# Performance work log

Hardware: AMD Instinct MI355X
Metric: run time of the kernel (lower is better)

## Reference

```python
import jax, jax.numpy as jnp
import numpy as np

SAMPLE_RATE = 44100
NUM_FILTERS = 3
FREQ_LO, FREQ_HI = 100.0, 3000.0
Q_LO, Q_HI = 1.0, 5.0
GAIN_LO, GAIN_HI = -24.0, 24.0


def _center_freqs():
    # power_ratio(i/N, f_lo, f_hi) = f_lo * (f_hi/f_lo)**(i/N)
    return [FREQ_LO * (FREQ_HI / FREQ_LO) ** (i / NUM_FILTERS) for i in range(NUM_FILTERS)]


def setup_inputs() -> dict:
    key = jax.random.key(0)
    k1, k2, k3 = jax.random.split(key, 3)
    audio = jax.random.normal(k1, (32, 441000), dtype=jnp.float32)  # [B, T]
    # Q sampled like power_ratio(u, q_lo, q_hi) = q_lo*(q_hi/q_lo)**u
    u = jax.random.uniform(k2, (NUM_FILTERS,), dtype=jnp.float32)
    qs = Q_LO * (Q_HI / Q_LO) ** u
    gains = jax.random.uniform(k3, (NUM_FILTERS,), dtype=jnp.float32,
                               minval=GAIN_LO, maxval=GAIN_HI)
    return {"audio": audio, "qs": qs, "gains": gains}


def _biquad(x, b0, b1, b2, a1, a2):
    """Direct-form-I biquad over time axis. x: [B, T]; coeffs normalized by a0."""
    B = x.shape[0]
    z = jnp.zeros((B,), x.dtype)

    def step(carry, xn):
        x1, x2, y1, y2 = carry
        yn = b0 * xn + b1 * x1 + b2 * x2 - a1 * y1 - a2 * y2
        return (xn, x1, yn, y1), yn

    _, y = jax.lax.scan(step, (z, z, z, z), x.T)  # scan over T
    return y.T


def _peaking_eq(audio, center_freq, gain, Q):
    # torchaudio.functional.equalizer_biquad coefficients
    w0 = 2.0 * jnp.pi * center_freq / SAMPLE_RATE
    alpha = jnp.sin(w0) / (2.0 * Q)
    A = jnp.exp(gain / 40.0 * jnp.log(10.0))  # 10**(gain/40)
    b0 = 1.0 + alpha * A
    b1 = -2.0 * jnp.cos(w0)
    b2 = 1.0 - alpha * A
    a0 = 1.0 + alpha / A
    a1 = -2.0 * jnp.cos(w0)
    a2 = 1.0 - alpha / A
    return _biquad(audio, b0 / a0, b1 / a0, b2 / a0, a1 / a0, a2 / a0)


def reference(audio, qs, gains):
    cfs = _center_freqs()
    for i in range(NUM_FILTERS):
        audio = _peaking_eq(audio, cfs[i], gains[i], qs[i])
    return audio
```

## Files before the change

### kernel.cpp

```cpp
#include <hip/hip_runtime.h>
#include <math.h>

#define SR      44100.0
#define T_LEN   441000
#define B_ROWS  32
#define CHUNK   32
#define NCH     13782
#define WPR     216
#define NWAVE   (B_ROWS * WPR)
#define NBLK    (NWAVE / 4)
#define NSEG    8
#define SEGCH   1724

#define WS_COEF 0
#define WS_W    16
#define WS_G    64
#define WS_V    128
#define WS_T    512
#define WS_E    2048
#define WS_F    1574912

typedef __attribute__((address_space(1))) const void gconst_t;
typedef __attribute__((address_space(3))) void lds_t;
#define GL2LDS(gp, lp) __builtin_amdgcn_global_load_lds((gconst_t*)(gp), (lds_t*)(lp), 16, 0, 0)


__device__ __forceinline__ void mm6(const double* X, const double* Y, double* Z, int t) {
  if (t < 36) {
    int i = t / 6, j = t % 6;
    double s = 0.0;
    #pragma unroll
    for (int k = 0; k < 6; k++) s += X[i*6+k] * Y[k*6+j];
    Z[t] = s;
  }
}

__global__ __launch_bounds__(64) void k0_setup(const float* __restrict__ qs,
                                               const float* __restrict__ gains,
                                               float* __restrict__ ws) {
  __shared__ double dco[3][5];
  __shared__ double M0[36], M1[36];
  __shared__ double Vd[10][36];
  int t = threadIdx.x;
  if (t < 3) {
    int f = t;
    double cf = 100.0 * exp(log(30.0) * (double)f / 3.0);
    double w0 = 2.0 * M_PI * cf / SR;
    double alpha = sin(w0) / (2.0 * (double)qs[f]);
    double Ag = exp((double)gains[f] * (2.302585092994045684 / 40.0));
    double a0 = 1.0 + alpha / Ag;
    dco[f][0] = (1.0 + alpha * Ag) / a0;
    dco[f][1] = (-2.0 * cos(w0)) / a0;
    dco[f][2] = (1.0 - alpha * Ag) / a0;
    dco[f][3] = (-2.0 * cos(w0)) / a0;
    dco[f][4] = (1.0 - alpha / Ag) / a0;
  }
  __syncthreads();
  if (t < 15) ws[WS_COEF + t] = (float)dco[t/5][t%5];
  if (t == 0) {
    double u[7] = {0,0,0,0,0,0,1};
    for (int f = 0; f < 3; f++) {
      double b0=dco[f][0], b1=dco[f][1], b2=dco[f][2], a1=dco[f][3], a2=dco[f][4];
      double yv[7], s1p[7], s2p[7];
      for (int i = 0; i < 7; i++) {
        yv[i]  = b0 * u[i] + ((i == 2*f)   ? 1.0 : 0.0);
        s1p[i] = b1 * u[i] + ((i == 2*f+1) ? 1.0 : 0.0) - a1 * yv[i];
        s2p[i] = b2 * u[i] - a2 * yv[i];
      }
      for (int i = 0; i < 6; i++) { M0[(2*f)*6+i] = s1p[i]; M0[(2*f+1)*6+i] = s2p[i]; }
      for (int i = 0; i < 7; i++) u[i] = yv[i];
    }
  }
  __syncthreads();
  double* cur = M0; double* oth = M1;
  for (int s = 0; s < 5; s++) {
    mm6(cur, cur, oth, t); __syncthreads();
    double* tm = cur; cur = oth; oth = tm;
  }
  if (t < 36) ws[WS_W + t] = (float)cur[t];
  mm6(cur, cur, Vd[0], t); __syncthreads();
  for (int k = 1; k < 10; k++) { mm6(Vd[k-1], Vd[k-1], Vd[k], t); __syncthreads(); }
  if (t < 36) for (int k = 0; k < 10; k++) ws[WS_V + k*36 + t] = (float)Vd[k][t];
  mm6(Vd[1], Vd[2], oth, t); __syncthreads();
  mm6(oth, Vd[3], cur, t); __syncthreads();
  mm6(cur, Vd[4], oth, t); __syncthreads();
  mm6(oth, Vd[6], cur, t); __syncthreads();
  mm6(cur, Vd[8], oth, t); __syncthreads();
  mm6(oth, Vd[9], cur, t); __syncthreads();
  if (t < 36) ws[WS_G + t] = (float)cur[t];
}


#define LOAD_COEFS(cf) \
  const float b00=cf[0],b10=cf[1],b20=cf[2],a10=cf[3],a20=cf[4]; \
  const float b01=cf[5],b11=cf[6],b21=cf[7],a11=cf[8],a21=cf[9]; \
  const float b02=cf[10],b12=cf[11],b22=cf[12],a12=cf[13],a22=cf[14];

#define CASCADE_STEP(xx) do { \
    float y1 = fmaf(b00, (xx), s11); \
    s11 = fmaf(-a10, y1, fmaf(b10, (xx), s21)); \
    s21 = fmaf(-a20, y1, b20 * (xx)); \
    float y2 = fmaf(b01, y1, s12); \
    s12 = fmaf(-a11, y2, fmaf(b11, y1, s22)); \
    s22 = fmaf(-a21, y2, b21 * y1); \
    y3 = fmaf(b02, y2, s13); \
    s13 = fmaf(-a12, y3, fmaf(b12, y2, s23)); \
    s23 = fmaf(-a22, y3, b22 * y2); \
  } while (0)



__global__ __launch_bounds__(256) void k1_states(const float* __restrict__ x,
                                                 float* __restrict__ ws) {
  __shared__ float lds[4 * 2048];
  int wib = threadIdx.x >> 6, lane = threadIdx.x & 63;
  int gw = blockIdx.x * 4 + wib;
  int row = gw / WPR, wci = gw % WPR;
  long rowbase = (long)row * T_LEN;
  int s0 = wci << 11;
  int span4 = (min(2048, T_LEN - s0)) >> 2;
  const float4* xp = (const float4*)(x + rowbase + s0);
  float* slab = lds + (wib << 11);
  if (span4 == 512) {
    #pragma unroll
    for (int i = 0; i < 8; i++) {
      int s = (i << 6) + lane;
      int g = (s & ~7) | ((s & 7) ^ ((s >> 3) & 7));
      GL2LDS(xp + g, slab + (i << 8));
    }
  } else {
    #pragma unroll
    for (int i = 0; i < 8; i++) {
      int s = (i << 6) + lane;
      int g = (s & ~7) | ((s & 7) ^ ((s >> 3) & 7));
      if (g < span4) GL2LDS(xp + g, slab + (i << 8));
    }
  }
  __syncthreads();
  int ci = (wci << 6) + lane;
  if (ci < NCH) {
    const float* cf = ws + WS_COEF;
    LOAD_COEFS(cf);
    int rem = min(CHUNK, T_LEN - (ci << 5));
    int n4 = rem >> 2;
    const float* rowp = slab + (lane << 5);
    int xr = lane & 7;
    float s11=0,s21=0,s12=0,s22=0,s13=0,s23=0, y3;
    if (n4 == 8) {
      #pragma unroll
      for (int j4 = 0; j4 < 8; j4++) {
        float4 v = *(const float4*)(rowp + ((j4 ^ xr) << 2));
        CASCADE_STEP(v.x); CASCADE_STEP(v.y); CASCADE_STEP(v.z); CASCADE_STEP(v.w);
      }
    } else {
      for (int j4 = 0; j4 < n4; j4++) {
        float4 v = *(const float4*)(rowp + ((j4 ^ xr) << 2));
        CASCADE_STEP(v.x); CASCADE_STEP(v.y); CASCADE_STEP(v.z); CASCADE_STEP(v.w);
      }
    }
    (void)y3;
    float* F = ws + WS_F + ((long)row * NCH + ci) * 6;
    F[0]=s11; F[1]=s21; F[2]=s12; F[3]=s22; F[4]=s13; F[5]=s23;
  }
}


__global__ __launch_bounds__(1024) void k2a(float* __restrict__ ws) {
  int seg = blockIdx.x & 7, row = blockIdx.x >> 3, t = threadIdx.x;
  __shared__ float bufA[1024][7], bufB[1024][7];
  __shared__ float sW[36], sV[10][36];
  for (int i = t; i < 36; i += 1024) sW[i] = ws[WS_W + i];
  for (int i = t; i < 360; i += 1024) sV[i/36][i%36] = ws[WS_V + i];
  int segstart = seg * SEGCH;
  int nch = min(SEGCH, NCH - segstart);
  int nact = nch >> 1;
  __syncthreads();
  const float* F = ws + WS_F + ((long)row * NCH + segstart) * 6;
  float v[6] = {0,0,0,0,0,0};
  if (t < nact) {
    #pragma unroll
    for (int c = 0; c < 2; c++) {
      const float* Fj = F + (long)(2*t + c) * 6;
      float nv[6];
      #pragma unroll
      for (int i = 0; i < 6; i++) {
        float s = Fj[i];
        #pragma unroll
        for (int k = 0; k < 6; k++) s = fmaf(sW[i*6+k], v[k], s);
        nv[i] = s;
      }
      #pragma unroll
      for (int i = 0; i < 6; i++) v[i] = nv[i];
    }
  }
  #pragma unroll
  for (int i = 0; i < 6; i++) bufA[t][i] = v[i];
  __syncthreads();
  float (*src)[7] = bufA, (*dst)[7] = bufB;
  for (int k = 0; k < 10; k++) {
    int d = 1 << k;
    float nv[6];
    if (t >= d) {
      #pragma unroll
      for (int i = 0; i < 6; i++) {
        float s = src[t][i];
        #pragma unroll
        for (int kk = 0; kk < 6; kk++) s = fmaf(sV[k][i*6+kk], src[t-d][kk], s);
        nv[i] = s;
      }
    } else {
      #pragma unroll
      for (int i = 0; i < 6; i++) nv[i] = src[t][i];
    }
    #pragma unroll
    for (int i = 0; i < 6; i++) dst[t][i] = nv[i];
    __syncthreads();
    float (*tm)[7] = src; src = dst; dst = tm;
  }
  float* Ep = ws + WS_E + ((long)blockIdx.x * 1024 + t) * 6;
  if (t > 0) {
    #pragma unroll
    for (int i = 0; i < 6; i++) Ep[i] = src[t-1][i];
  } else {
    #pragma unroll
    for (int i = 0; i < 6; i++) Ep[i] = 0.0f;
  }
  if (t == nact - 1) {
    float* Tp = ws + WS_T + (long)blockIdx.x * 6;
    #pragma unroll
    for (int i = 0; i < 6; i++) Tp[i] = src[t][i];
  }
}


__global__ __launch_bounds__(1024) void k2c(float* __restrict__ ws) {
  int seg = blockIdx.x & 7, row = blockIdx.x >> 3, t = threadIdx.x;
  __shared__ float sW[36], sG[36], sV[10][36], sT[8][6], sO[6];
  for (int i = t; i < 36; i += 1024) { sW[i] = ws[WS_W + i]; sG[i] = ws[WS_G + i]; }
  for (int i = t; i < 360; i += 1024) sV[i/36][i%36] = ws[WS_V + i];
  if (t < 48) sT[t/6][t%6] = ws[WS_T + ((long)(row*8) + t/6) * 6 + t%6];
  __syncthreads();
  if (t == 0) {
    float o[6] = {0,0,0,0,0,0};
    for (int s2 = 0; s2 < seg; s2++) {
      float no[6];
      #pragma unroll
      for (int i = 0; i < 6; i++) {
        float s = sT[s2][i];
        #pragma unroll
        for (int k = 0; k < 6; k++) s = fmaf(sG[i*6+k], o[k], s);
        no[i] = s;
      }
      #pragma unroll
      for (int i = 0; i < 6; i++) o[i] = no[i];
    }
    #pragma unroll
    for (int i = 0; i < 6; i++) sO[i] = o[i];
  }
  __syncthreads();
  int segstart = seg * SEGCH;
  int nch = min(SEGCH, NCH - segstart);
  int nact = nch >> 1;
  if (t < nact) {
    float e[6];
    #pragma unroll
    for (int i = 0; i < 6; i++) e[i] = sO[i];
    for (int k = 0; k < 10; k++) {
      if ((t >> k) & 1) {
        float ne[6];
        #pragma unroll
        for (int i = 0; i < 6; i++) {
          float s = 0.0f;
          #pragma unroll
          for (int kk = 0; kk < 6; kk++) s = fmaf(sV[k][i*6+kk], e[kk], s);
          ne[i] = s;
        }
        #pragma unroll
        for (int i = 0; i < 6; i++) e[i] = ne[i];
      }
    }
    const float* Er = ws + WS_E + ((long)blockIdx.x * 1024 + t) * 6;
    #pragma unroll
    for (int i = 0; i < 6; i++) e[i] += Er[i];
    float* Fj = ws + WS_F + ((long)row * NCH + segstart + 2*t) * 6;
    #pragma unroll
    for (int c = 0; c < 2; c++) {
      float nv[6];
      #pragma unroll
      for (int i = 0; i < 6; i++) {
        float s = Fj[c*6 + i];
        #pragma unroll
        for (int k = 0; k < 6; k++) s = fmaf(sW[i*6+k], e[k], s);
        nv[i] = s;
      }
      #pragma unroll
      for (int i = 0; i < 6; i++) { Fj[c*6 + i] = e[i]; e[i] = nv[i]; }
    }
  }
}


__global__ __launch_bounds__(256) void k3_emit(const float* __restrict__ x,
                                               float* __restrict__ y,
                                               const float* __restrict__ ws) {
  __shared__ float lds[4 * 2048];
  int wib = threadIdx.x >> 6, lane = threadIdx.x & 63;
  int gw = blockIdx.x * 4 + wib;
  int row = gw / WPR, wci = gw % WPR;
  long rowbase = (long)row * T_LEN;
  int s0 = wci << 11;
  int span4 = (min(2048, T_LEN - s0)) >> 2;
  const float4* xp = (const float4*)(x + rowbase + s0);
  float* slab = lds + (wib << 11);
  if (span4 == 512) {
    #pragma unroll
    for (int i = 0; i < 8; i++) {
      int s = (i << 6) + lane;
      int g = (s & ~7) | ((s & 7) ^ ((s >> 3) & 7));
      GL2LDS(xp + g, slab + (i << 8));
    }
  } else {
    #pragma unroll
    for (int i = 0; i < 8; i++) {
      int s = (i << 6) + lane;
      int g = (s & ~7) | ((s & 7) ^ ((s >> 3) & 7));
      if (g < span4) GL2LDS(xp + g, slab + (i << 8));
    }
  }
  int ci = (wci << 6) + lane;
  float e0=0,e1=0,e2=0,e3=0,e4=0,e5=0;
  if (ci < NCH) {
    const float* E = ws + WS_F + ((long)row * NCH + ci) * 6;
    e0=E[0]; e1=E[1]; e2=E[2]; e3=E[3]; e4=E[4]; e5=E[5];
  }
  __syncthreads();
  if (ci < NCH) {
    const float* cf = ws + WS_COEF;
    LOAD_COEFS(cf);
    float s11=e0, s21=e1, s12=e2, s22=e3, s13=e4, s23=e5;
    int rem = min(CHUNK, T_LEN - (ci << 5));
    int n4 = rem >> 2;
    float* rowp = slab + (lane << 5);
    int xr = lane & 7;
    float y3;
    if (n4 == 8) {
      #pragma unroll
      for (int j4 = 0; j4 < 8; j4++) {
        float* p = rowp + ((j4 ^ xr) << 2);
        float4 v = *(const float4*)p;
        float4 o;
        CASCADE_STEP(v.x); o.x = y3;
        CASCADE_STEP(v.y); o.y = y3;
        CASCADE_STEP(v.z); o.z = y3;
        CASCADE_STEP(v.w); o.w = y3;
        *(float4*)p = o;
      }
    } else {
      for (int j4 = 0; j4 < n4; j4++) {
        float* p = rowp + ((j4 ^ xr) << 2);
        float4 v = *(const float4*)p;
        float4 o;
        CASCADE_STEP(v.x); o.x = y3;
        CASCADE_STEP(v.y); o.y = y3;
        CASCADE_STEP(v.z); o.z = y3;
        CASCADE_STEP(v.w); o.w = y3;
        *(float4*)p = o;
      }
    }
  }
  __syncthreads();
  float4* yp = (float4*)(y + rowbase + s0);
  if (span4 == 512) {
    #pragma unroll
    for (int i = 0; i < 8; i++) {
      int g = (i << 6) + lane;
      int s = (g & ~7) | ((g & 7) ^ ((g >> 3) & 7));
      yp[g] = *(const float4*)(slab + (s << 2));
    }
  } else {
    #pragma unroll
    for (int i = 0; i < 8; i++) {
      int g = (i << 6) + lane;
      int s = (g & ~7) | ((g & 7) ^ ((g >> 3) & 7));
      if (g < span4) yp[g] = *(const float4*)(slab + (s << 2));
    }
  }
}

extern "C" void kernel_launch(void* const* d_in, const int* in_sizes, int n_in,
                              void* d_out, int out_size, void* d_ws, size_t ws_size,
                              hipStream_t stream) {
  const float* audio = (const float*)d_in[0];
  const float* qs    = (const float*)d_in[1];
  const float* gains = (const float*)d_in[2];
  float* out = (float*)d_out;
  float* ws  = (float*)d_ws;

  hipLaunchKernelGGL(k0_setup, dim3(1), dim3(64), 0, stream, qs, gains, ws);
  hipLaunchKernelGGL(k1_states, dim3(NBLK), dim3(256), 0, stream, audio, ws);
  hipLaunchKernelGGL(k2a, dim3(B_ROWS * NSEG), dim3(1024), 0, stream, ws);
  hipLaunchKernelGGL(k2c, dim3(B_ROWS * NSEG), dim3(1024), 0, stream, ws);
  hipLaunchKernelGGL(k3_emit, dim3(NBLK), dim3(256), 0, stream, audio, out, ws);
}
```

Baseline: 64.98 us.

## Collapse five-kernel pipeline to three by fusing setup and per-row scan

Removes the separate setup kernel: the biquad coefficients are now recomputed per block in the state and emit kernels, and the transition-matrix powers are computed inside the scan kernel. The two segmented scan kernels are merged into one kernel with one block per row, where each thread serially folds 14 chunks, runs a 10-round Hillis-Steele scan, then writes the corrected states back. This cuts two kernel launches and the cross-segment fixup. In exchange only 32 blocks run the scan, with longer serial per-thread loops and redundant double-precision matrix setup in every block.

```diff
diff --git a/kernel.cpp b/kernel.cpp
--- a/kernel.cpp
+++ b/kernel.cpp
@@ -9,87 +9,31 @@
 #define WPR     216
 #define NWAVE   (B_ROWS * WPR)
 #define NBLK    (NWAVE / 4)
-#define NSEG    8
-#define SEGCH   1724
-
-#define WS_COEF 0
-#define WS_W    16
-#define WS_G    64
-#define WS_V    128
-#define WS_T    512
-#define WS_E    2048
-#define WS_F    1574912
+#define SPAN    14
+#define ROUNDS  10
+
+#define WS_F    0
 
 typedef __attribute__((address_space(1))) const void gconst_t;
 typedef __attribute__((address_space(3))) void lds_t;
 #define GL2LDS(gp, lp) __builtin_amdgcn_global_load_lds((gconst_t*)(gp), (lds_t*)(lp), 16, 0, 0)
 
 
-__device__ __forceinline__ void mm6(const double* X, const double* Y, double* Z, int t) {
-  if (t < 36) {
-    int i = t / 6, j = t % 6;
-    double s = 0.0;
-    #pragma unroll
-    for (int k = 0; k < 6; k++) s += X[i*6+k] * Y[k*6+j];
-    Z[t] = s;
-  }
-}
-
-__global__ __launch_bounds__(64) void k0_setup(const float* __restrict__ qs,
-                                               const float* __restrict__ gains,
-                                               float* __restrict__ ws) {
-  __shared__ double dco[3][5];
-  __shared__ double M0[36], M1[36];
-  __shared__ double Vd[10][36];
-  int t = threadIdx.x;
-  if (t < 3) {
-    int f = t;
-    double cf = 100.0 * exp(log(30.0) * (double)f / 3.0);
-    double w0 = 2.0 * M_PI * cf / SR;
-    double alpha = sin(w0) / (2.0 * (double)qs[f]);
-    double Ag = exp((double)gains[f] * (2.302585092994045684 / 40.0));
-    double a0 = 1.0 + alpha / Ag;
-    dco[f][0] = (1.0 + alpha * Ag) / a0;
-    dco[f][1] = (-2.0 * cos(w0)) / a0;
-    dco[f][2] = (1.0 - alpha * Ag) / a0;
-    dco[f][3] = (-2.0 * cos(w0)) / a0;
-    dco[f][4] = (1.0 - alpha / Ag) / a0;
-  }
-  __syncthreads();
-  if (t < 15) ws[WS_COEF + t] = (float)dco[t/5][t%5];
-  if (t == 0) {
-    double u[7] = {0,0,0,0,0,0,1};
-    for (int f = 0; f < 3; f++) {
-      double b0=dco[f][0], b1=dco[f][1], b2=dco[f][2], a1=dco[f][3], a2=dco[f][4];
-      double yv[7], s1p[7], s2p[7];
-      for (int i = 0; i < 7; i++) {
-        yv[i]  = b0 * u[i] + ((i == 2*f)   ? 1.0 : 0.0);
-        s1p[i] = b1 * u[i] + ((i == 2*f+1) ? 1.0 : 0.0) - a1 * yv[i];
-        s2p[i] = b2 * u[i] - a2 * yv[i];
-      }
-      for (int i = 0; i < 6; i++) { M0[(2*f)*6+i] = s1p[i]; M0[(2*f+1)*6+i] = s2p[i]; }
-      for (int i = 0; i < 7; i++) u[i] = yv[i];
-    }
-  }
-  __syncthreads();
-  double* cur = M0; double* oth = M1;
-  for (int s = 0; s < 5; s++) {
-    mm6(cur, cur, oth, t); __syncthreads();
-    double* tm = cur; cur = oth; oth = tm;
-  }
-  if (t < 36) ws[WS_W + t] = (float)cur[t];
-  mm6(cur, cur, Vd[0], t); __syncthreads();
-  for (int k = 1; k < 10; k++) { mm6(Vd[k-1], Vd[k-1], Vd[k], t); __syncthreads(); }
-  if (t < 36) for (int k = 0; k < 10; k++) ws[WS_V + k*36 + t] = (float)Vd[k][t];
-  mm6(Vd[1], Vd[2], oth, t); __syncthreads();
-  mm6(oth, Vd[3], cur, t); __syncthreads();
-  mm6(cur, Vd[4], oth, t); __syncthreads();
-  mm6(oth, Vd[6], cur, t); __syncthreads();
-  mm6(cur, Vd[8], oth, t); __syncthreads();
-  mm6(oth, Vd[9], cur, t); __syncthreads();
-  if (t < 36) ws[WS_G + t] = (float)cur[t];
-}
-
+#define COMPUTE_COEFS_TO_LDS(scoef, qs, gains) do { \
+    if (threadIdx.x < 3) { \
+      int f = threadIdx.x; \
+      double cfq = 100.0 * exp(log(30.0) * (double)f / 3.0); \
+      double w0 = 2.0 * M_PI * cfq / SR; \
+      double alpha = sin(w0) / (2.0 * (double)qs[f]); \
+      double Ag = exp((double)gains[f] * (2.302585092994045684 / 40.0)); \
+      double a0 = 1.0 + alpha / Ag; \
+      scoef[f*5+0] = (float)((1.0 + alpha * Ag) / a0); \
+      scoef[f*5+1] = (float)((-2.0 * cos(w0)) / a0); \
+      scoef[f*5+2] = (float)((1.0 - alpha * Ag) / a0); \
+      scoef[f*5+3] = (float)((-2.0 * cos(w0)) / a0); \
+      scoef[f*5+4] = (float)((1.0 - alpha / Ag) / a0); \
+    } \
+  } while (0)
 
 #define LOAD_COEFS(cf) \
   const float b00=cf[0],b10=cf[1],b20=cf[2],a10=cf[3],a20=cf[4]; \
@@ -110,9 +54,12 @@
 
 
 
-__global__ __launch_bounds__(256) void k1_states(const float* __restrict__ x,
+__global__ __launch_bounds__(256) void kA_states(const float* __restrict__ x,
+                                                 const float* __restrict__ qs,
+                                                 const float* __restrict__ gains,
                                                  float* __restrict__ ws) {
   __shared__ float lds[4 * 2048];
+  __shared__ float scoef[16];
   int wib = threadIdx.x >> 6, lane = threadIdx.x & 63;
   int gw = blockIdx.x * 4 + wib;
   int row = gw / WPR, wci = gw % WPR;
@@ -136,11 +83,11 @@
       if (g < span4) GL2LDS(xp + g, slab + (i << 8));
     }
   }
+  COMPUTE_COEFS_TO_LDS(scoef, qs, gains);
   __syncthreads();
   int ci = (wci << 6) + lane;
   if (ci < NCH) {
-    const float* cf = ws + WS_COEF;
-    LOAD_COEFS(cf);
+    LOAD_COEFS(scoef);
     int rem = min(CHUNK, T_LEN - (ci << 5));
     int n4 = rem >> 2;
     const float* rowp = slab + (lane << 5);
@@ -165,39 +112,95 @@
 }
 
 
-__global__ __launch_bounds__(1024) void k2a(float* __restrict__ ws) {
-  int seg = blockIdx.x & 7, row = blockIdx.x >> 3, t = threadIdx.x;
+__device__ __forceinline__ void mm6d(const double* X, const double* Y, double* Z, int t) {
+  if (t < 36) {
+    int i = t / 6, j = t % 6;
+    double s = 0.0;
+    #pragma unroll
+    for (int k = 0; k < 6; k++) s += X[i*6+k] * Y[k*6+j];
+    Z[t] = s;
+  }
+}
+
+__global__ __launch_bounds__(1024) void kB_scan(const float* __restrict__ qs,
+                                                const float* __restrict__ gains,
+                                                float* __restrict__ ws) {
+  int row = blockIdx.x, t = threadIdx.x;
+  __shared__ double Da[36], Db[36], Dc[36], Dd[36];
+  __shared__ float sW[36], sV[ROUNDS][36];
   __shared__ float bufA[1024][7], bufB[1024][7];
-  __shared__ float sW[36], sV[10][36];
-  for (int i = t; i < 36; i += 1024) sW[i] = ws[WS_W + i];
-  for (int i = t; i < 360; i += 1024) sV[i/36][i%36] = ws[WS_V + i];
-  int segstart = seg * SEGCH;
-  int nch = min(SEGCH, NCH - segstart);
-  int nact = nch >> 1;
-  __syncthreads();
-  const float* F = ws + WS_F + ((long)row * NCH + segstart) * 6;
+
+  if (t == 0) {
+    double dco[3][5];
+    for (int f = 0; f < 3; f++) {
+      double cfq = 100.0 * exp(log(30.0) * (double)f / 3.0);
+      double w0 = 2.0 * M_PI * cfq / SR;
+      double alpha = sin(w0) / (2.0 * (double)qs[f]);
+      double Ag = exp((double)gains[f] * (2.302585092994045684 / 40.0));
+      double a0 = 1.0 + alpha / Ag;
+      dco[f][0] = (1.0 + alpha * Ag) / a0;
+      dco[f][1] = (-2.0 * cos(w0)) / a0;
+      dco[f][2] = (1.0 - alpha * Ag) / a0;
+      dco[f][3] = (-2.0 * cos(w0)) / a0;
+      dco[f][4] = (1.0 - alpha / Ag) / a0;
+    }
+    double u[7] = {0,0,0,0,0,0,1};
+    for (int f = 0; f < 3; f++) {
+      double b0=dco[f][0], b1=dco[f][1], b2=dco[f][2], a1=dco[f][3], a2=dco[f][4];
+      double yv[7], s1p[7], s2p[7];
+      for (int i = 0; i < 7; i++) {
+        yv[i]  = b0 * u[i] + ((i == 2*f)   ? 1.0 : 0.0);
+        s1p[i] = b1 * u[i] + ((i == 2*f+1) ? 1.0 : 0.0) - a1 * yv[i];
+        s2p[i] = b2 * u[i] - a2 * yv[i];
+      }
+      for (int i = 0; i < 6; i++) { Da[(2*f)*6+i] = s1p[i]; Da[(2*f+1)*6+i] = s2p[i]; }
+      for (int i = 0; i < 7; i++) u[i] = yv[i];
+    }
+  }
+  __syncthreads();
+  mm6d(Da, Da, Db, t); __syncthreads();
+  mm6d(Db, Db, Da, t); __syncthreads();
+  mm6d(Da, Da, Db, t); __syncthreads();
+  mm6d(Db, Db, Da, t); __syncthreads();
+  mm6d(Da, Da, Db, t); __syncthreads();
+  if (t < 36) sW[t] = (float)Db[t];
+  mm6d(Db, Db, Da, t); __syncthreads();
+  mm6d(Db, Da, Dc, t); __syncthreads();
+  mm6d(Da, Da, Dd, t); __syncthreads();
+  mm6d(Dc, Dd, Da, t); __syncthreads();
+  mm6d(Da, Da, Dc, t); __syncthreads();
+  if (t < 36) sV[0][t] = (float)Dc[t];
+  {
+    double* cur = Dc; double* oth = Dd;
+    for (int k = 1; k < ROUNDS; k++) {
+      mm6d(cur, cur, oth, t); __syncthreads();
+      if (t < 36) sV[k][t] = (float)oth[t];
+      double* tm = cur; cur = oth; oth = tm;
+    }
+  }
+  __syncthreads();
+
+  float* F = ws + WS_F + (long)row * NCH * 6;
+  int j0 = t * SPAN, j1 = min(j0 + SPAN, NCH);
   float v[6] = {0,0,0,0,0,0};
-  if (t < nact) {
-    #pragma unroll
-    for (int c = 0; c < 2; c++) {
-      const float* Fj = F + (long)(2*t + c) * 6;
-      float nv[6];
-      #pragma unroll
-      for (int i = 0; i < 6; i++) {
-        float s = Fj[i];
-        #pragma unroll
-        for (int k = 0; k < 6; k++) s = fmaf(sW[i*6+k], v[k], s);
-        nv[i] = s;
-      }
-      #pragma unroll
-      for (int i = 0; i < 6; i++) v[i] = nv[i];
-    }
+  for (int j = j0; j < j1; j++) {
+    const float* Fj = F + (long)j * 6;
+    float nv[6];
+    #pragma unroll
+    for (int i = 0; i < 6; i++) {
+      float s = Fj[i];
+      #pragma unroll
+      for (int k = 0; k < 6; k++) s = fmaf(sW[i*6+k], v[k], s);
+      nv[i] = s;
+    }
+    #pragma unroll
+    for (int i = 0; i < 6; i++) v[i] = nv[i];
   }
   #pragma unroll
   for (int i = 0; i < 6; i++) bufA[t][i] = v[i];
   __syncthreads();
   float (*src)[7] = bufA, (*dst)[7] = bufB;
-  for (int k = 0; k < 10; k++) {
+  for (int k = 0; k < ROUNDS; k++) {
     int d = 1 << k;
     float nv[6];
     if (t >= d) {
@@ -217,93 +220,32 @@
     __syncthreads();
     float (*tm)[7] = src; src = dst; dst = tm;
   }
-  float* Ep = ws + WS_E + ((long)blockIdx.x * 1024 + t) * 6;
-  if (t > 0) {
-    #pragma unroll
-    for (int i = 0; i < 6; i++) Ep[i] = src[t-1][i];
-  } else {
-    #pragma unroll
-    for (int i = 0; i < 6; i++) Ep[i] = 0.0f;
-  }
-  if (t == nact - 1) {
-    float* Tp = ws + WS_T + (long)blockIdx.x * 6;
-    #pragma unroll
-    for (int i = 0; i < 6; i++) Tp[i] = src[t][i];
-  }
-}
-
-
-__global__ __launch_bounds__(1024) void k2c(float* __restrict__ ws) {
-  int seg = blockIdx.x & 7, row = blockIdx.x >> 3, t = threadIdx.x;
-  __shared__ float sW[36], sG[36], sV[10][36], sT[8][6], sO[6];
-  for (int i = t; i < 36; i += 1024) { sW[i] = ws[WS_W + i]; sG[i] = ws[WS_G + i]; }
-  for (int i = t; i < 360; i += 1024) sV[i/36][i%36] = ws[WS_V + i];
-  if (t < 48) sT[t/6][t%6] = ws[WS_T + ((long)(row*8) + t/6) * 6 + t%6];
-  __syncthreads();
-  if (t == 0) {
-    float o[6] = {0,0,0,0,0,0};
-    for (int s2 = 0; s2 < seg; s2++) {
-      float no[6];
-      #pragma unroll
-      for (int i = 0; i < 6; i++) {
-        float s = sT[s2][i];
-        #pragma unroll
-        for (int k = 0; k < 6; k++) s = fmaf(sG[i*6+k], o[k], s);
-        no[i] = s;
-      }
-      #pragma unroll
-      for (int i = 0; i < 6; i++) o[i] = no[i];
-    }
-    #pragma unroll
-    for (int i = 0; i < 6; i++) sO[i] = o[i];
-  }
-  __syncthreads();
-  int segstart = seg * SEGCH;
-  int nch = min(SEGCH, NCH - segstart);
-  int nact = nch >> 1;
-  if (t < nact) {
-    float e[6];
-    #pragma unroll
-    for (int i = 0; i < 6; i++) e[i] = sO[i];
-    for (int k = 0; k < 10; k++) {
-      if ((t >> k) & 1) {
-        float ne[6];
-        #pragma unroll
-        for (int i = 0; i < 6; i++) {
-          float s = 0.0f;
-          #pragma unroll
-          for (int kk = 0; kk < 6; kk++) s = fmaf(sV[k][i*6+kk], e[kk], s);
-          ne[i] = s;
-        }
-        #pragma unroll
-        for (int i = 0; i < 6; i++) e[i] = ne[i];
-      }
-    }
-    const float* Er = ws + WS_E + ((long)blockIdx.x * 1024 + t) * 6;
-    #pragma unroll
-    for (int i = 0; i < 6; i++) e[i] += Er[i];
-    float* Fj = ws + WS_F + ((long)row * NCH + segstart + 2*t) * 6;
-    #pragma unroll
-    for (int c = 0; c < 2; c++) {
-      float nv[6];
-      #pragma unroll
-      for (int i = 0; i < 6; i++) {
-        float s = Fj[c*6 + i];
-        #pragma unroll
-        for (int k = 0; k < 6; k++) s = fmaf(sW[i*6+k], e[k], s);
-        nv[i] = s;
-      }
-      #pragma unroll
-      for (int i = 0; i < 6; i++) { Fj[c*6 + i] = e[i]; e[i] = nv[i]; }
-    }
-  }
-}
-
-
-__global__ __launch_bounds__(256) void k3_emit(const float* __restrict__ x,
+  float e[6];
+  if (t > 0) { for (int i = 0; i < 6; i++) e[i] = src[t-1][i]; }
+  else       { for (int i = 0; i < 6; i++) e[i] = 0.0f; }
+  for (int j = j0; j < j1; j++) {
+    float* Fj = F + (long)j * 6;
+    float nv[6];
+    #pragma unroll
+    for (int i = 0; i < 6; i++) {
+      float s = Fj[i];
+      #pragma unroll
+      for (int k = 0; k < 6; k++) s = fmaf(sW[i*6+k], e[k], s);
+      nv[i] = s;
+    }
+    #pragma unroll
+    for (int i = 0; i < 6; i++) { Fj[i] = e[i]; e[i] = nv[i]; }
+  }
+}
+
+
+__global__ __launch_bounds__(256) void kC_emit(const float* __restrict__ x,
+                                               const float* __restrict__ qs,
+                                               const float* __restrict__ gains,
                                                float* __restrict__ y,
                                                const float* __restrict__ ws) {
   __shared__ float lds[4 * 2048];
+  __shared__ float scoef[16];
   int wib = threadIdx.x >> 6, lane = threadIdx.x & 63;
   int gw = blockIdx.x * 4 + wib;
   int row = gw / WPR, wci = gw % WPR;
@@ -327,6 +269,7 @@
       if (g < span4) GL2LDS(xp + g, slab + (i << 8));
     }
   }
+  COMPUTE_COEFS_TO_LDS(scoef, qs, gains);
   int ci = (wci << 6) + lane;
   float e0=0,e1=0,e2=0,e3=0,e4=0,e5=0;
   if (ci < NCH) {
@@ -335,8 +278,7 @@
   }
   __syncthreads();
   if (ci < NCH) {
-    const float* cf = ws + WS_COEF;
-    LOAD_COEFS(cf);
+    LOAD_COEFS(scoef);
     float s11=e0, s21=e1, s12=e2, s22=e3, s13=e4, s23=e5;
     int rem = min(CHUNK, T_LEN - (ci << 5));
     int n4 = rem >> 2;
@@ -396,9 +338,7 @@
   float* out = (float*)d_out;
   float* ws  = (float*)d_ws;
 
-  hipLaunchKernelGGL(k0_setup, dim3(1), dim3(64), 0, stream, qs, gains, ws);
-  hipLaunchKernelGGL(k1_states, dim3(NBLK), dim3(256), 0, stream, audio, ws);
-  hipLaunchKernelGGL(k2a, dim3(B_ROWS * NSEG), dim3(1024), 0, stream, ws);
-  hipLaunchKernelGGL(k2c, dim3(B_ROWS * NSEG), dim3(1024), 0, stream, ws);
-  hipLaunchKernelGGL(k3_emit, dim3(NBLK), dim3(256), 0, stream, audio, out, ws);
-}
+  hipLaunchKernelGGL(kA_states, dim3(NBLK), dim3(256), 0, stream, audio, qs, gains, ws);
+  hipLaunchKernelGGL(kB_scan, dim3(B_ROWS), dim3(1024), 0, stream, qs, gains, ws);
+  hipLaunchKernelGGL(kC_emit, dim3(NBLK), dim3(256), 0, stream, audio, qs, gains, out, ws);
+}
```

New measurement: 100.2 us. 1.54x slower.
